# Optimization experiments

Measured on AMD Instinct MI355X. Metric: run time of the kernel, lower is better.

## Reference

```python
import jax, jax.numpy as jnp
import numpy as np

N = 50000
E = 800000
IN = 256
H = 8
D = 32
NEG_SLOPE = 0.2


def setup_inputs() -> dict:
    key = jax.random.key(0)
    ks = jax.random.split(key, 16)
    inp = {
        "h": jax.random.normal(ks[0], (N, IN), jnp.float32),
        "src_a": jax.random.randint(ks[1], (E,), 0, N),
        "dst_a": jax.random.randint(ks[2], (E,), 0, N),
        "src_b": jax.random.randint(ks[3], (E,), 0, N),
        "dst_b": jax.random.randint(ks[4], (E,), 0, N),
        "W_a": jax.random.normal(ks[5], (IN, H * D), jnp.float32) * 0.05,
        "attn_l_a": jax.random.normal(ks[6], (H, D), jnp.float32) * 0.1,
        "attn_r_a": jax.random.normal(ks[7], (H, D), jnp.float32) * 0.1,
        "bias_a": jax.random.normal(ks[8], (H * D,), jnp.float32) * 0.1,
        "W_b": jax.random.normal(ks[9], (IN, H * D), jnp.float32) * 0.05,
        "attn_l_b": jax.random.normal(ks[10], (H, D), jnp.float32) * 0.1,
        "attn_r_b": jax.random.normal(ks[11], (H, D), jnp.float32) * 0.1,
        "bias_b": jax.random.normal(ks[12], (H * D,), jnp.float32) * 0.1,
        "sem_W1": jax.random.normal(ks[13], (H * D, 128), jnp.float32) * 0.05,
        "sem_b1": jnp.zeros((128,), jnp.float32),
        "sem_W2": jax.random.normal(ks[14], (128, 1), jnp.float32) * 0.1,
    }
    return inp


def gat_conv(h, src, dst, W, attn_l, attn_r, bias):
    # DGL GATConv: project, per-edge additive attention, segment softmax over dst, scatter-agg, bias, ELU
    feat = (h @ W).reshape(N, H, D)                      # [N,H,D]
    el = (feat * attn_l).sum(-1)                          # [N,H]
    er = (feat * attn_r).sum(-1)                          # [N,H]
    e = el[src] + er[dst]                                 # [E,H]
    e = jnp.where(e > 0, e, NEG_SLOPE * e)                # LeakyReLU(0.2)
    m = jax.ops.segment_max(e, dst, num_segments=N)       # [N,H] (-inf for empty)
    ex = jnp.exp(e - m[dst])                              # [E,H]
    denom = jax.ops.segment_sum(ex, dst, num_segments=N)  # [N,H]
    msg = feat[src] * ex[:, :, None]                      # [E,H,D]
    agg = jax.ops.segment_sum(msg, dst, num_segments=N)   # [N,H,D]
    safe = jnp.where(denom > 0, denom, 1.0)
    rst = agg / safe[:, :, None] + bias.reshape(1, H, D)
    rst = jnp.where(rst > 0, rst, jnp.expm1(rst))         # ELU
    return rst.reshape(N, H * D)


def semantic_attention(z, sem_W1, sem_b1, sem_W2):
    # z: [N, M, H*D]
    w = (jnp.tanh(z @ sem_W1 + sem_b1) @ sem_W2).mean(0)  # [M,1]
    beta = jax.nn.softmax(w, axis=0)                      # [M,1]
    return (beta[None] * z).sum(1)                        # [N, H*D]


def reference(h, src_a, dst_a, src_b, dst_b,
              W_a, attn_l_a, attn_r_a, bias_a,
              W_b, attn_l_b, attn_r_b, bias_b,
              sem_W1, sem_b1, sem_W2):
    z_a = gat_conv(h, src_a, dst_a, W_a, attn_l_a, attn_r_a, bias_a)
    z_b = gat_conv(h, src_b, dst_b, W_b, attn_l_b, attn_r_b, bias_b)
    z = jnp.stack([z_a, z_b], axis=1)                     # [N,2,H*D]
    return semantic_attention(z, sem_W1, sem_b1, sem_W2)
```

## Files before the change

kernel.cpp:

```cpp
#include <hip/hip_runtime.h>
#include <math.h>

typedef __attribute__((ext_vector_type(8))) short bf16x8;
typedef __attribute__((ext_vector_type(4))) float f32x4;
typedef __attribute__((ext_vector_type(4))) unsigned short us4;
typedef __attribute__((ext_vector_type(8))) unsigned short us8;

static constexpr int kN  = 50000;
static constexpr int kE  = 800000;
static constexpr int kNBUK = 98;
static constexpr int kCAP  = 9216;

__device__ __forceinline__ float b2f(unsigned short u) {
  union { unsigned u; float f; } x; x.u = ((unsigned)u) << 16; return x.f;
}
__device__ __forceinline__ unsigned short f2b(float f) {
  union { float f; unsigned u; } x; x.f = f;
  unsigned u = x.u;
  unsigned r = (u + 0x7fffu + ((u >> 16) & 1u)) >> 16;
  return (unsigned short)r;
}

__global__ __launch_bounds__(256)
void k_prep(const float* __restrict__ Wa, const float* __restrict__ Wb,
            const float* __restrict__ W1,
            unsigned short* __restrict__ wta, unsigned short* __restrict__ wtb,
            unsigned short* __restrict__ w1t) {
  int b = blockIdx.x, t = threadIdx.x;
  if (b < 256) {
    int i = b * 256 + t, j = i >> 8, k = i & 255;
    wta[j * 256 + k] = f2b(Wa[k * 256 + j]);
  } else if (b < 512) {
    int i = (b - 256) * 256 + t, j = i >> 8, k = i & 255;
    wtb[j * 256 + k] = f2b(Wb[k * 256 + j]);
  } else {
    int i = (b - 512) * 256 + t, j = i >> 8, k = i & 255;
    w1t[j * 256 + k] = f2b(W1[k * 128 + j]);
  }
}

__global__ __launch_bounds__(512, 4)
void k_gemm(const float* __restrict__ h,
            const unsigned short* __restrict__ wta,
            const unsigned short* __restrict__ wtb,
            const float* __restrict__ ala, const float* __restrict__ ara,
            const float* __restrict__ alb, const float* __restrict__ arb,
            unsigned short* __restrict__ fa, unsigned short* __restrict__ fb,
            float* __restrict__ ela, float* __restrict__ era,
            float* __restrict__ elb, float* __restrict__ erb) {
  __shared__ us8 la[128 * 8];
  __shared__ us8 lb[256 * 8];
  const int z = blockIdx.y;
  const unsigned short* wt = z ? wtb : wta;
  unsigned short* f = z ? fb : fa;
  const float* al = z ? alb : ala;
  const float* ar = z ? arb : ara;
  float* el = z ? elb : ela;
  float* er = z ? erb : era;
  const int m0 = blockIdx.x * 128;
  const int t = threadIdx.x;
  const int lane = t & 63;
  const int wave = t >> 6;
  const int col = lane & 15;
  const int quad = lane >> 4;
  const int mw = (wave >> 2) * 64;
  const int nw = (wave & 3) * 64;
  f32x4 acc[4][4];
#pragma unroll
  for (int i = 0; i < 4; ++i)
#pragma unroll
    for (int j = 0; j < 4; ++j) acc[i][j] = (f32x4){0.f, 0.f, 0.f, 0.f};

  for (int ks = 0; ks < 4; ++ks) {
    const int k0 = ks * 64;
    __syncthreads();
#pragma unroll
    for (int i = 0; i < 4; ++i) {
      int idx = i * 512 + t;
      int r = idx >> 4, g = (idx >> 1) & 7, half = idx & 1;
      int gr = m0 + r;
      f32x4 v = {0.f, 0.f, 0.f, 0.f};
      if (gr < kN) v = *(const f32x4*)(h + (size_t)gr * 256 + k0 + g * 8 + half * 4);
      us4 o;
      o.x = f2b(v.x); o.y = f2b(v.y); o.z = f2b(v.z); o.w = f2b(v.w);
      *(us4*)((unsigned short*)&la[r * 8 + (g ^ (r & 7))] + half * 4) = o;
    }
#pragma unroll
    for (int i = 0; i < 4; ++i) {
      int idx = i * 512 + t;
      int r = idx >> 3, g = idx & 7;
      lb[r * 8 + (g ^ (r & 7))] = *(const us8*)(wt + r * 256 + k0 + g * 8);
    }
    __syncthreads();
#pragma unroll
    for (int k32 = 0; k32 < 64; k32 += 32) {
      const int cg = (k32 >> 3) + quad;
      bf16x8 af[4], bf[4];
#pragma unroll
      for (int s = 0; s < 4; ++s) {
        int arow = mw + s * 16 + col;
        af[s] = (bf16x8)la[arow * 8 + (cg ^ (arow & 7))];
        int brow = nw + s * 16 + col;
        bf[s] = (bf16x8)lb[brow * 8 + (cg ^ (brow & 7))];
      }
#pragma unroll
      for (int i = 0; i < 4; ++i)
#pragma unroll
        for (int j = 0; j < 4; ++j)
          acc[i][j] = __builtin_amdgcn_mfma_f32_16x16x32_bf16(af[i], bf[j],
                                                              acc[i][j], 0, 0, 0);
    }
  }
#pragma unroll
  for (int i = 0; i < 4; ++i) {
#pragma unroll
    for (int r = 0; r < 4; ++r) {
      int row = m0 + mw + i * 16 + quad * 4 + r;
      if (row < kN) {
#pragma unroll
        for (int j = 0; j < 4; ++j)
          f[(size_t)row * 256 + nw + j * 16 + col] = f2b(acc[i][j][r]);
      }
    }
  }
  float alv[4], arv[4];
#pragma unroll
  for (int j = 0; j < 4; ++j) {
    alv[j] = al[nw + j * 16 + col];
    arv[j] = ar[nw + j * 16 + col];
  }
  const int hA = nw >> 5;
#pragma unroll
  for (int i = 0; i < 4; ++i) {
#pragma unroll
    for (int r = 0; r < 4; ++r) {
      float pAl = acc[i][0][r] * alv[0] + acc[i][1][r] * alv[1];
      float pBl = acc[i][2][r] * alv[2] + acc[i][3][r] * alv[3];
      float pAr = acc[i][0][r] * arv[0] + acc[i][1][r] * arv[1];
      float pBr = acc[i][2][r] * arv[2] + acc[i][3][r] * arv[3];
#pragma unroll
      for (int off = 1; off < 16; off <<= 1) {
        pAl += __shfl_xor(pAl, off);
        pBl += __shfl_xor(pBl, off);
        pAr += __shfl_xor(pAr, off);
        pBr += __shfl_xor(pBr, off);
      }
      int row = m0 + mw + i * 16 + quad * 4 + r;
      if (col == 0 && row < kN) {
        el[row * 8 + hA] = pAl;
        el[row * 8 + hA + 1] = pBl;
        er[row * 8 + hA] = pAr;
        er[row * 8 + hA + 1] = pBr;
      }
    }
  }
}

__global__ __launch_bounds__(256)
void k_part(const int* __restrict__ sa, const int* __restrict__ da,
            const int* __restrict__ sb, const int* __restrict__ db,
            int* __restrict__ cnt, unsigned* __restrict__ pay) {
  int y = blockIdx.y;
  const int* s = y ? sb : sa;
  const int* d = y ? db : da;
  unsigned* p = pay + (size_t)y * kNBUK * kCAP;
  int* cn = cnt + y * kNBUK;
  __shared__ unsigned stash[6400];
  __shared__ int h[kNBUK];
  int t = threadIdx.x;
  if (t < kNBUK) h[t] = 0;
  __syncthreads();
  int e0 = blockIdx.x * 6400;
#pragma unroll 5
  for (int it = 0; it < 25; ++it) {
    int e = e0 + it * 256 + t;
    int sv = s[e], dv = d[e];
    int b = dv >> 9;
    stash[it * 256 + t] = (unsigned)sv | ((unsigned)(dv & 511) << 16) |
                          ((unsigned)b << 25);
    atomicAdd(&h[b], 1);
  }
  __syncthreads();
  if (t < kNBUK) h[t] = atomicAdd(&cn[t], h[t]);
  __syncthreads();
#pragma unroll 5
  for (int it = 0; it < 25; ++it) {
    unsigned w = stash[it * 256 + t];
    int b = w >> 25;
    int slot = atomicAdd(&h[b], 1);
    p[b * kCAP + slot] = w & 0x1FFFFFFu;
  }
}

__global__ __launch_bounds__(256)
void k_bscan(const int* __restrict__ cnt, int* __restrict__ bbase,
             int* __restrict__ rpa, int* __restrict__ rpb) {
  __shared__ int buf[2][128];
  int t = threadIdx.x;
  int y = t >> 7, i = t & 127;
  int x = (i < kNBUK) ? cnt[y * kNBUK + i] : 0;
  buf[y][i] = x;
  __syncthreads();
  for (int off = 1; off < 128; off <<= 1) {
    int v = (i >= off) ? buf[y][i - off] : 0;
    __syncthreads();
    buf[y][i] += v;
    __syncthreads();
  }
  if (i < kNBUK) bbase[y * kNBUK + i] = buf[y][i] - x;
  if (t == 0) { rpa[kN] = kE; rpb[kN] = kE; }
}

__global__ __launch_bounds__(256)
void k_bucket(const int* __restrict__ cnt, const int* __restrict__ bbase,
              const unsigned* __restrict__ pay,
              int* __restrict__ rpa, int* __restrict__ rpb,
              int* __restrict__ esa, int* __restrict__ esb) {
  int b = blockIdx.x, y = blockIdx.y;
  int* rp = y ? rpb : rpa;
  int* es = y ? esb : esa;
  const unsigned* p = pay + ((size_t)y * kNBUK + b) * kCAP;
  int c = cnt[y * kNBUK + b];
  int base = bbase[y * kNBUK + b];
  __shared__ unsigned pl[kCAP];
  __shared__ int h[512];
  __shared__ int buf[256];
  int t = threadIdx.x;
  h[t] = 0; h[t + 256] = 0;
  __syncthreads();
  for (int i = t; i < c; i += 256) {
    unsigned w = p[i];
    pl[i] = w;
    atomicAdd(&h[(w >> 16) & 511], 1);
  }
  __syncthreads();
  int a = h[2 * t], b1 = h[2 * t + 1];
  int s2 = a + b1;
  buf[t] = s2;
  __syncthreads();
  for (int off = 1; off < 256; off <<= 1) {
    int v = (t >= off) ? buf[t - off] : 0;
    __syncthreads();
    buf[t] += v;
    __syncthreads();
  }
  int ex = buf[t] - s2;
  int g0 = b * 512 + 2 * t;
  if (g0 < kN) rp[g0] = base + ex;
  if (g0 + 1 < kN) rp[g0 + 1] = base + ex + a;
  h[2 * t] = ex;
  h[2 * t + 1] = ex + a;
  __syncthreads();
  for (int i = t; i < c; i += 256) {
    unsigned w = pl[i];
    int slot = atomicAdd(&h[(w >> 16) & 511], 1);
    es[base + slot] = (int)(w & 0xFFFFu);
  }
}

__global__ __launch_bounds__(256)
void k_agg(const int* __restrict__ rpa, const int* __restrict__ rpb,
           const int* __restrict__ esa, const int* __restrict__ esb,
           const float* __restrict__ ela, const float* __restrict__ era,
           const float* __restrict__ elb, const float* __restrict__ erb,
           const unsigned short* __restrict__ fa,
           const unsigned short* __restrict__ fb,
           const float* __restrict__ biasa, const float* __restrict__ biasb,
           float* __restrict__ za, unsigned short* __restrict__ zb) {
  __shared__ float wls[4][512];
  __shared__ int sls[4][64];
  int bx = blockIdx.x;
  int y = bx >= 12500;
  int nb = y ? bx - 12500 : bx;
  const int* rp = y ? rpb : rpa;
  const int* es = y ? esb : esa;
  const float* el = y ? elb : ela;
  const float* er = y ? erb : era;
  const unsigned short* feat = y ? fb : fa;
  const float* bias = y ? biasb : biasa;
  int lane = threadIdx.x & 63;
  int wave = threadIdx.x >> 6;
  int n = nb * 4 + wave;
  int hh = lane >> 3;
  int h = lane & 7;
  unsigned idxb = (unsigned)lane * 8u;
  float erh = er[n * 8 + h];
  int e0 = rp[n], e1 = rp[n + 1];
  float dsum = 0.f;
  float a0 = 0.f, a1 = 0.f, a2 = 0.f, a3 = 0.f;

  for (int cb = e0; cb < e1; cb += 64) {
    int cnt = e1 - cb;
    if (cnt > 64) cnt = 64;
    for (int it = 0; it * 8 < cnt; ++it) {
      int j = it * 8 + hh;
      if (j < cnt) {
        int s = es[cb + j];
        float ev = *(const float*)((const char*)el + ((unsigned)s << 5) +
                                   ((unsigned)h << 2)) + erh;
        ev = fmaxf(ev, 0.2f * ev);
        float w = __expf(ev);
        wls[wave][it * 64 + lane] = w;
        if (h == 0) sls[wave][j] = s;
        dsum += w;
      }
    }
    int j = 0;
    for (; j + 3 < cnt; j += 4) {
      int s0 = sls[wave][j], s1 = sls[wave][j + 1];
      int s2 = sls[wave][j + 2], s3 = sls[wave][j + 3];
      float w0 = wls[wave][j * 8 + hh];
      float w1 = wls[wave][j * 8 + 8 + hh];
      float w2 = wls[wave][j * 8 + 16 + hh];
      float w3 = wls[wave][j * 8 + 24 + hh];
      us4 f0 = *(const us4*)((const char*)feat + (((unsigned)s0 << 9) + idxb));
      us4 f1 = *(const us4*)((const char*)feat + (((unsigned)s1 << 9) + idxb));
      us4 f2 = *(const us4*)((const char*)feat + (((unsigned)s2 << 9) + idxb));
      us4 f3 = *(const us4*)((const char*)feat + (((unsigned)s3 << 9) + idxb));
      a0 += w0 * b2f(f0.x) + w1 * b2f(f1.x) + w2 * b2f(f2.x) + w3 * b2f(f3.x);
      a1 += w0 * b2f(f0.y) + w1 * b2f(f1.y) + w2 * b2f(f2.y) + w3 * b2f(f3.y);
      a2 += w0 * b2f(f0.z) + w1 * b2f(f1.z) + w2 * b2f(f2.z) + w3 * b2f(f3.z);
      a3 += w0 * b2f(f0.w) + w1 * b2f(f1.w) + w2 * b2f(f2.w) + w3 * b2f(f3.w);
    }
    for (; j < cnt; ++j) {
      int s0 = sls[wave][j];
      float w0 = wls[wave][j * 8 + hh];
      us4 f0 = *(const us4*)((const char*)feat + (((unsigned)s0 << 9) + idxb));
      a0 += w0 * b2f(f0.x);
      a1 += w0 * b2f(f0.y);
      a2 += w0 * b2f(f0.z);
      a3 += w0 * b2f(f0.w);
    }
  }
  dsum += __shfl_xor(dsum, 8);
  dsum += __shfl_xor(dsum, 16);
  dsum += __shfl_xor(dsum, 32);
  float dh = __shfl(dsum, hh);
  float inv = 1.f / (dh > 0.f ? dh : 1.f);
  f32x4 b4 = *(const f32x4*)(bias + lane * 4);
  float r0 = a0 * inv + b4.x;
  float r1 = a1 * inv + b4.y;
  float r2 = a2 * inv + b4.z;
  float r3 = a3 * inv + b4.w;
  r0 = r0 > 0.f ? r0 : expm1f(r0);
  r1 = r1 > 0.f ? r1 : expm1f(r1);
  r2 = r2 > 0.f ? r2 : expm1f(r2);
  r3 = r3 > 0.f ? r3 : expm1f(r3);
  if (y == 0) {
    f32x4 o = {r0, r1, r2, r3};
    *(f32x4*)(za + n * 256 + lane * 4) = o;
  } else {
    us4 o;
    o.x = f2b(r0); o.y = f2b(r1); o.z = f2b(r2); o.w = f2b(r3);
    *(us4*)(zb + n * 256 + lane * 4) = o;
  }
}

__global__ __launch_bounds__(256)
void k_sem(const float* __restrict__ za,
           const unsigned short* __restrict__ zb,
           const unsigned short* __restrict__ w1t,
           const float* __restrict__ b1,
           const float* __restrict__ W2,
           float* __restrict__ wacc) {
  __shared__ us8 w1l[4096];
  int t = threadIdx.x;
  for (int i = t; i < 4096; i += 256) {
    int j = i >> 5, c = i & 31;
    w1l[j * 32 + (c ^ (j & 7))] = ((const us8*)w1t)[i];
  }
  __syncthreads();
  int lane = t & 63, wave = t >> 6;
  int col = lane & 15, quad = lane >> 4;
  float b1v[8], w2v[8];
#pragma unroll
  for (int tt = 0; tt < 8; ++tt) {
    b1v[tt] = b1[tt * 16 + col];
    w2v[tt] = W2[tt * 16 + col];
  }
  int gw = blockIdx.x * 4 + wave;
  int nw = gridDim.x * 4;
  float sa = 0.f, sb = 0.f;
  for (int gt = gw; gt < 6250; gt += nw) {
    f32x4 acc[8];
#pragma unroll
    for (int tt = 0; tt < 8; ++tt) acc[tt] = (f32x4){0.f, 0.f, 0.f, 0.f};
#pragma unroll
    for (int ks = 0; ks < 8; ++ks) {
      bf16x8 a;
      if (gt < 3125) {
        const float* ap = za + (size_t)gt * 4096 + col * 256 + ks * 32 + quad * 8;
        f32x4 a0 = *(const f32x4*)ap;
        f32x4 a1 = *(const f32x4*)(ap + 4);
        a[0] = (short)f2b(a0.x); a[1] = (short)f2b(a0.y);
        a[2] = (short)f2b(a0.z); a[3] = (short)f2b(a0.w);
        a[4] = (short)f2b(a1.x); a[5] = (short)f2b(a1.y);
        a[6] = (short)f2b(a1.z); a[7] = (short)f2b(a1.w);
      } else {
        a = *(const bf16x8*)(zb + (size_t)(gt - 3125) * 4096 + col * 256 +
                             ks * 32 + quad * 8);
      }
      int c = ks * 4 + quad;
#pragma unroll
      for (int tt = 0; tt < 8; ++tt) {
        int j = tt * 16 + col;
        bf16x8 b = (bf16x8)w1l[j * 32 + (c ^ (j & 7))];
        acc[tt] = __builtin_amdgcn_mfma_f32_16x16x32_bf16(a, b, acc[tt], 0, 0, 0);
      }
    }
    float tot = 0.f;
#pragma unroll
    for (int tt = 0; tt < 8; ++tt)
#pragma unroll
      for (int r = 0; r < 4; ++r)
        tot += tanhf(acc[tt][r] + b1v[tt]) * w2v[tt];
#pragma unroll
    for (int off = 1; off < 64; off <<= 1) tot += __shfl_xor(tot, off);
    if (gt < 3125) sa += tot; else sb += tot;
  }
  if (lane == 0) {
    if (sa != 0.f) atomicAdd(&wacc[0], sa);
    if (sb != 0.f) atomicAdd(&wacc[1], sb);
  }
}

__global__ __launch_bounds__(256)
void k_combine(const float* __restrict__ za,
               const unsigned short* __restrict__ zb,
               const float* __restrict__ wacc,
               float* __restrict__ out) {
  int i = blockIdx.x * 256 + threadIdx.x;
  float wa = wacc[0] * (1.f / kN), wb = wacc[1] * (1.f / kN);
  float mx = fmaxf(wa, wb);
  float ea = __expf(wa - mx), eb = __expf(wb - mx);
  float inv = 1.f / (ea + eb);
  float ba = ea * inv, bb = eb * inv;
  f32x4 x = ((const f32x4*)za)[i];
  us4 yv = ((const us4*)zb)[i];
  f32x4 o;
#pragma unroll
  for (int j = 0; j < 4; ++j)
    o[j] = ba * x[j] + bb * b2f(yv[j]);
  ((f32x4*)out)[i] = o;
}

extern "C" void kernel_launch(void* const* d_in, const int* in_sizes, int n_in,
                              void* d_out, int out_size, void* d_ws, size_t ws_size,
                              hipStream_t stream) {
  const float* hin = (const float*)d_in[0];
  const int* src_a = (const int*)d_in[1];
  const int* dst_a = (const int*)d_in[2];
  const int* src_b = (const int*)d_in[3];
  const int* dst_b = (const int*)d_in[4];
  const float* W_a = (const float*)d_in[5];
  const float* al_a = (const float*)d_in[6];
  const float* ar_a = (const float*)d_in[7];
  const float* bias_a = (const float*)d_in[8];
  const float* W_b = (const float*)d_in[9];
  const float* al_b = (const float*)d_in[10];
  const float* ar_b = (const float*)d_in[11];
  const float* bias_b = (const float*)d_in[12];
  const float* sW1 = (const float*)d_in[13];
  const float* sb1 = (const float*)d_in[14];
  const float* sW2 = (const float*)d_in[15];
  float* out = (float*)d_out;

  char* wsb = (char*)d_ws;
  size_t off = 0;
  auto alloc = [&](size_t bytes) -> char* {
    char* p = wsb + off;
    off = (off + bytes + 511) & ~(size_t)511;
    return p;
  };
  unsigned short* feat_a = (unsigned short*)alloc((size_t)kN * 256 * 2);
  unsigned short* feat_b = (unsigned short*)alloc((size_t)kN * 256 * 2);
  unsigned short* z_b    = (unsigned short*)alloc((size_t)kN * 256 * 2);
  float* el_a = (float*)alloc((size_t)kN * 8 * 4);
  float* er_a = (float*)alloc((size_t)kN * 8 * 4);
  float* el_b = (float*)alloc((size_t)kN * 8 * 4);
  float* er_b = (float*)alloc((size_t)kN * 8 * 4);
  unsigned short* wt_a = (unsigned short*)alloc(65536 * 2);
  unsigned short* wt_b = (unsigned short*)alloc(65536 * 2);
  unsigned short* w1t  = (unsigned short*)alloc(32768 * 2);
  int* rp_a = (int*)alloc((size_t)(kN + 1) * 4);
  int* rp_b = (int*)alloc((size_t)(kN + 1) * 4);
  int* es_a = (int*)alloc((size_t)kE * 4);
  int* es_b = (int*)alloc((size_t)kE * 4);
  unsigned* pay = (unsigned*)alloc((size_t)2 * kNBUK * kCAP * 4);
  int* cnt = (int*)alloc((size_t)2 * kNBUK * 4);
  int* bbase = (int*)alloc((size_t)2 * kNBUK * 4);
  float* wacc = (float*)alloc(2 * 4);

  hipMemsetAsync(cnt, 0, (size_t)2 * kNBUK * 4, stream);
  hipMemsetAsync(wacc, 0, 8, stream);

  k_prep<<<640, 256, 0, stream>>>(W_a, W_b, sW1, wt_a, wt_b, w1t);
  k_part<<<dim3(125, 2), 256, 0, stream>>>(src_a, dst_a, src_b, dst_b, cnt, pay);
  k_bscan<<<1, 256, 0, stream>>>(cnt, bbase, rp_a, rp_b);
  k_bucket<<<dim3(kNBUK, 2), 256, 0, stream>>>(cnt, bbase, pay,
                                               rp_a, rp_b, es_a, es_b);
  k_gemm<<<dim3(391, 2), 512, 0, stream>>>(hin, wt_a, wt_b,
                                           al_a, ar_a, al_b, ar_b,
                                           feat_a, feat_b,
                                           el_a, er_a, el_b, er_b);
  k_agg<<<25000, 256, 0, stream>>>(rp_a, rp_b, es_a, es_b,
                                   el_a, er_a, el_b, er_b,
                                   feat_a, feat_b, bias_a, bias_b,
                                   out, z_b);
  k_sem<<<512, 256, 0, stream>>>(out, z_b, w1t, sb1, sW2, wacc);
  k_combine<<<12500, 256, 0, stream>>>(out, z_b, wacc, out);
}
```

Before: 453.0 us.

## Widen feature gathers to 16-byte loads with half-wave edge split; use fast tanh/rcp

```diff
diff --git a/kernel.cpp b/kernel.cpp
--- a/kernel.cpp
+++ b/kernel.cpp
@@ -283,11 +283,15 @@
   int n = nb * 4 + wave;
   int hh = lane >> 3;
   int h = lane & 7;
-  unsigned idxb = (unsigned)lane * 8u;
+  int half = lane >> 5;
+  int l5 = lane & 31;
+  int h2 = l5 >> 2;
+  unsigned idx16 = (unsigned)l5 * 16u;
   float erh = er[n * 8 + h];
   int e0 = rp[n], e1 = rp[n + 1];
   float dsum = 0.f;
   float a0 = 0.f, a1 = 0.f, a2 = 0.f, a3 = 0.f;
+  float a4 = 0.f, a5 = 0.f, a6 = 0.f, a7 = 0.f;
 
   for (int cb = e0; cb < e1; cb += 64) {
     int cnt = e1 - cb;
@@ -306,53 +310,79 @@
       }
     }
     int j = 0;
-    for (; j + 3 < cnt; j += 4) {
-      int s0 = sls[wave][j], s1 = sls[wave][j + 1];
-      int s2 = sls[wave][j + 2], s3 = sls[wave][j + 3];
-      float w0 = wls[wave][j * 8 + hh];
-      float w1 = wls[wave][j * 8 + 8 + hh];
-      float w2 = wls[wave][j * 8 + 16 + hh];
-      float w3 = wls[wave][j * 8 + 24 + hh];
-      us4 f0 = *(const us4*)((const char*)feat + (((unsigned)s0 << 9) + idxb));
-      us4 f1 = *(const us4*)((const char*)feat + (((unsigned)s1 << 9) + idxb));
-      us4 f2 = *(const us4*)((const char*)feat + (((unsigned)s2 << 9) + idxb));
-      us4 f3 = *(const us4*)((const char*)feat + (((unsigned)s3 << 9) + idxb));
-      a0 += w0 * b2f(f0.x) + w1 * b2f(f1.x) + w2 * b2f(f2.x) + w3 * b2f(f3.x);
-      a1 += w0 * b2f(f0.y) + w1 * b2f(f1.y) + w2 * b2f(f2.y) + w3 * b2f(f3.y);
-      a2 += w0 * b2f(f0.z) + w1 * b2f(f1.z) + w2 * b2f(f2.z) + w3 * b2f(f3.z);
-      a3 += w0 * b2f(f0.w) + w1 * b2f(f1.w) + w2 * b2f(f2.w) + w3 * b2f(f3.w);
-    }
-    for (; j < cnt; ++j) {
-      int s0 = sls[wave][j];
-      float w0 = wls[wave][j * 8 + hh];
-      us4 f0 = *(const us4*)((const char*)feat + (((unsigned)s0 << 9) + idxb));
-      a0 += w0 * b2f(f0.x);
-      a1 += w0 * b2f(f0.y);
-      a2 += w0 * b2f(f0.z);
-      a3 += w0 * b2f(f0.w);
-    }
-  }
+    for (; j + 7 < cnt; j += 8) {
+#pragma unroll
+      for (int p = 0; p < 4; ++p) {
+        int jj = j + 2 * p + half;
+        int s = sls[wave][jj];
+        float w = wls[wave][jj * 8 + h2];
+        us8 fv = *(const us8*)((const char*)feat + (((unsigned)s << 9) + idx16));
+        a0 += w * b2f(fv[0]);
+        a1 += w * b2f(fv[1]);
+        a2 += w * b2f(fv[2]);
+        a3 += w * b2f(fv[3]);
+        a4 += w * b2f(fv[4]);
+        a5 += w * b2f(fv[5]);
+        a6 += w * b2f(fv[6]);
+        a7 += w * b2f(fv[7]);
+      }
+    }
+    if (j < cnt) {
+#pragma unroll
+      for (int p = 0; p < 4; ++p) {
+        int jj = j + 2 * p + half;
+        bool v = jj < cnt;
+        int jc = v ? jj : j;
+        int s = sls[wave][jc];
+        float w = v ? wls[wave][jc * 8 + h2] : 0.f;
+        us8 fv = *(const us8*)((const char*)feat + (((unsigned)s << 9) + idx16));
+        a0 += w * b2f(fv[0]);
+        a1 += w * b2f(fv[1]);
+        a2 += w * b2f(fv[2]);
+        a3 += w * b2f(fv[3]);
+        a4 += w * b2f(fv[4]);
+        a5 += w * b2f(fv[5]);
+        a6 += w * b2f(fv[6]);
+        a7 += w * b2f(fv[7]);
+      }
+    }
+  }
+  a0 += __shfl_xor(a0, 32); a1 += __shfl_xor(a1, 32);
+  a2 += __shfl_xor(a2, 32); a3 += __shfl_xor(a3, 32);
+  a4 += __shfl_xor(a4, 32); a5 += __shfl_xor(a5, 32);
+  a6 += __shfl_xor(a6, 32); a7 += __shfl_xor(a7, 32);
   dsum += __shfl_xor(dsum, 8);
   dsum += __shfl_xor(dsum, 16);
   dsum += __shfl_xor(dsum, 32);
-  float dh = __shfl(dsum, hh);
-  float inv = 1.f / (dh > 0.f ? dh : 1.f);
-  f32x4 b4 = *(const f32x4*)(bias + lane * 4);
-  float r0 = a0 * inv + b4.x;
-  float r1 = a1 * inv + b4.y;
-  float r2 = a2 * inv + b4.z;
-  float r3 = a3 * inv + b4.w;
-  r0 = r0 > 0.f ? r0 : expm1f(r0);
-  r1 = r1 > 0.f ? r1 : expm1f(r1);
-  r2 = r2 > 0.f ? r2 : expm1f(r2);
-  r3 = r3 > 0.f ? r3 : expm1f(r3);
+  float dh = __shfl(dsum, h2);
+  float inv = __builtin_amdgcn_rcpf(dh > 0.f ? dh : 1.f);
+  f32x4 blo = *(const f32x4*)(bias + l5 * 8);
+  f32x4 bhi = *(const f32x4*)(bias + l5 * 8 + 4);
+  float r0 = a0 * inv + blo.x;
+  float r1 = a1 * inv + blo.y;
+  float r2 = a2 * inv + blo.z;
+  float r3 = a3 * inv + blo.w;
+  float r4 = a4 * inv + bhi.x;
+  float r5 = a5 * inv + bhi.y;
+  float r6 = a6 * inv + bhi.z;
+  float r7 = a7 * inv + bhi.w;
+  r0 = r0 > 0.f ? r0 : __expf(r0) - 1.f;
+  r1 = r1 > 0.f ? r1 : __expf(r1) - 1.f;
+  r2 = r2 > 0.f ? r2 : __expf(r2) - 1.f;
+  r3 = r3 > 0.f ? r3 : __expf(r3) - 1.f;
+  r4 = r4 > 0.f ? r4 : __expf(r4) - 1.f;
+  r5 = r5 > 0.f ? r5 : __expf(r5) - 1.f;
+  r6 = r6 > 0.f ? r6 : __expf(r6) - 1.f;
+  r7 = r7 > 0.f ? r7 : __expf(r7) - 1.f;
+  f32x4 lo = {r0, r1, r2, r3};
+  f32x4 hi = {r4, r5, r6, r7};
+  f32x4 ov = half ? hi : lo;
   if (y == 0) {
-    f32x4 o = {r0, r1, r2, r3};
-    *(f32x4*)(za + n * 256 + lane * 4) = o;
+    *(f32x4*)((char*)za + (size_t)n * 1024 + l5 * 32 + half * 16) = ov;
   } else {
     us4 o;
-    o.x = f2b(r0); o.y = f2b(r1); o.z = f2b(r2); o.w = f2b(r3);
-    *(us4*)(zb + n * 256 + lane * 4) = o;
+    o.x = f2b(ov.x); o.y = f2b(ov.y); o.z = f2b(ov.z); o.w = f2b(ov.w);
+    *(us4*)((char*)zb + (size_t)n * 512 + l5 * 16 + half * 8) = o;
   }
 }
 
@@ -412,8 +442,12 @@
 #pragma unroll
     for (int tt = 0; tt < 8; ++tt)
 #pragma unroll
-      for (int r = 0; r < 4; ++r)
-        tot += tanhf(acc[tt][r] + b1v[tt]) * w2v[tt];
+      for (int r = 0; r < 4; ++r) {
+        float x = acc[tt][r] + b1v[tt];
+        x = fminf(fmaxf(x, -10.f), 10.f);
+        float ex = __expf(2.f * x);
+        tot += (ex - 1.f) * __builtin_amdgcn_rcpf(ex + 1.f) * w2v[tt];
+      }
 #pragma unroll
     for (int off = 1; off < 64; off <<= 1) tot += __shfl_xor(tot, off);
     if (gt < 3125) sa += tot; else sb += tot;
@@ -433,7 +467,7 @@
   float wa = wacc[0] * (1.f / kN), wb = wacc[1] * (1.f / kN);
   float mx = fmaxf(wa, wb);
   float ea = __expf(wa - mx), eb = __expf(wb - mx);
-  float inv = 1.f / (ea + eb);
+  float inv = __builtin_amdgcn_rcpf(ea + eb);
   float ba = ea * inv, bb = eb * inv;
   f32x4 x = ((const f32x4*)za)[i];
   us4 yv = ((const us4*)zb)[i];
```

Result: no change. 447.3 us (-1.2%).

## Process two destination nodes per wave with 16-byte feature gathers in aggregation

Applied to the files above, without the earlier changes.

```diff
diff --git a/kernel.cpp b/kernel.cpp
--- a/kernel.cpp
+++ b/kernel.cpp
@@ -267,11 +267,11 @@
            const unsigned short* __restrict__ fb,
            const float* __restrict__ biasa, const float* __restrict__ biasb,
            float* __restrict__ za, unsigned short* __restrict__ zb) {
-  __shared__ float wls[4][512];
-  __shared__ int sls[4][64];
+  __shared__ float wls[4][2][256];
+  __shared__ int sls[4][2][32];
   int bx = blockIdx.x;
-  int y = bx >= 12500;
-  int nb = y ? bx - 12500 : bx;
+  int y = bx >= 6250;
+  int nb = y ? bx - 6250 : bx;
   const int* rp = y ? rpb : rpa;
   const int* es = y ? esb : esa;
   const float* el = y ? elb : ela;
@@ -280,79 +280,166 @@
   const float* bias = y ? biasb : biasa;
   int lane = threadIdx.x & 63;
   int wave = threadIdx.x >> 6;
-  int n = nb * 4 + wave;
+  int nA = nb * 8 + wave * 2;
+  int nB = nA + 1;
   int hh = lane >> 3;
   int h = lane & 7;
-  unsigned idxb = (unsigned)lane * 8u;
-  float erh = er[n * 8 + h];
-  int e0 = rp[n], e1 = rp[n + 1];
-  float dsum = 0.f;
-  float a0 = 0.f, a1 = 0.f, a2 = 0.f, a3 = 0.f;
-
-  for (int cb = e0; cb < e1; cb += 64) {
-    int cnt = e1 - cb;
-    if (cnt > 64) cnt = 64;
-    for (int it = 0; it * 8 < cnt; ++it) {
+  int half = lane >> 5;
+  int l5 = lane & 31;
+  int h2 = l5 >> 2;
+  unsigned idx16 = (unsigned)l5 * 16u;
+  float erhA = er[nA * 8 + h];
+  float erhB = er[nB * 8 + h];
+  int e0A = rp[nA], e1A = rp[nA + 1], e1B = rp[nB + 1];
+  int cbA = e0A, cbB = e1A;
+  float dsumA = 0.f, dsumB = 0.f;
+  float aA0 = 0.f, aA1 = 0.f, aA2 = 0.f, aA3 = 0.f;
+  float aA4 = 0.f, aA5 = 0.f, aA6 = 0.f, aA7 = 0.f;
+  float aB0 = 0.f, aB1 = 0.f, aB2 = 0.f, aB3 = 0.f;
+  float aB4 = 0.f, aB5 = 0.f, aB6 = 0.f, aB7 = 0.f;
+
+  while (cbA < e1A || cbB < e1B) {
+    int cntA = e1A - cbA; cntA = cntA < 0 ? 0 : (cntA > 32 ? 32 : cntA);
+    int cntB = e1B - cbB; cntB = cntB < 0 ? 0 : (cntB > 32 ? 32 : cntB);
+#pragma unroll
+    for (int it = 0; it < 4; ++it) {
       int j = it * 8 + hh;
-      if (j < cnt) {
-        int s = es[cb + j];
-        float ev = *(const float*)((const char*)el + ((unsigned)s << 5) +
-                                   ((unsigned)h << 2)) + erh;
-        ev = fmaxf(ev, 0.2f * ev);
-        float w = __expf(ev);
-        wls[wave][it * 64 + lane] = w;
-        if (h == 0) sls[wave][j] = s;
-        dsum += w;
-      }
-    }
-    int j = 0;
-    for (; j + 3 < cnt; j += 4) {
-      int s0 = sls[wave][j], s1 = sls[wave][j + 1];
-      int s2 = sls[wave][j + 2], s3 = sls[wave][j + 3];
-      float w0 = wls[wave][j * 8 + hh];
-      float w1 = wls[wave][j * 8 + 8 + hh];
-      float w2 = wls[wave][j * 8 + 16 + hh];
-      float w3 = wls[wave][j * 8 + 24 + hh];
-      us4 f0 = *(const us4*)((const char*)feat + (((unsigned)s0 << 9) + idxb));
-      us4 f1 = *(const us4*)((const char*)feat + (((unsigned)s1 << 9) + idxb));
-      us4 f2 = *(const us4*)((const char*)feat + (((unsigned)s2 << 9) + idxb));
-      us4 f3 = *(const us4*)((const char*)feat + (((unsigned)s3 << 9) + idxb));
-      a0 += w0 * b2f(f0.x) + w1 * b2f(f1.x) + w2 * b2f(f2.x) + w3 * b2f(f3.x);
-      a1 += w0 * b2f(f0.y) + w1 * b2f(f1.y) + w2 * b2f(f2.y) + w3 * b2f(f3.y);
-      a2 += w0 * b2f(f0.z) + w1 * b2f(f1.z) + w2 * b2f(f2.z) + w3 * b2f(f3.z);
-      a3 += w0 * b2f(f0.w) + w1 * b2f(f1.w) + w2 * b2f(f2.w) + w3 * b2f(f3.w);
-    }
-    for (; j < cnt; ++j) {
-      int s0 = sls[wave][j];
-      float w0 = wls[wave][j * 8 + hh];
-      us4 f0 = *(const us4*)((const char*)feat + (((unsigned)s0 << 9) + idxb));
-      a0 += w0 * b2f(f0.x);
-      a1 += w0 * b2f(f0.y);
-      a2 += w0 * b2f(f0.z);
-      a3 += w0 * b2f(f0.w);
-    }
-  }
-  dsum += __shfl_xor(dsum, 8);
-  dsum += __shfl_xor(dsum, 16);
-  dsum += __shfl_xor(dsum, 32);
-  float dh = __shfl(dsum, hh);
-  float inv = 1.f / (dh > 0.f ? dh : 1.f);
-  f32x4 b4 = *(const f32x4*)(bias + lane * 4);
-  float r0 = a0 * inv + b4.x;
-  float r1 = a1 * inv + b4.y;
-  float r2 = a2 * inv + b4.z;
-  float r3 = a3 * inv + b4.w;
-  r0 = r0 > 0.f ? r0 : expm1f(r0);
-  r1 = r1 > 0.f ? r1 : expm1f(r1);
-  r2 = r2 > 0.f ? r2 : expm1f(r2);
-  r3 = r3 > 0.f ? r3 : expm1f(r3);
+      bool vA = j < cntA, vB = j < cntB;
+      int sA = vA ? es[cbA + j] : 0;
+      int sB = vB ? es[cbB + j] : 0;
+      float xA = vA ? *(const float*)((const char*)el + ((unsigned)sA << 5) +
+                                      ((unsigned)h << 2)) : 0.f;
+      float xB = vB ? *(const float*)((const char*)el + ((unsigned)sB << 5) +
+                                      ((unsigned)h << 2)) : 0.f;
+      float eA = xA + erhA, eB = xB + erhB;
+      eA = fmaxf(eA, 0.2f * eA);
+      eB = fmaxf(eB, 0.2f * eB);
+      float wA = __expf(eA), wB = __expf(eB);
+      wls[wave][0][it * 64 + lane] = wA;
+      wls[wave][1][it * 64 + lane] = wB;
+      if (vA) dsumA += wA;
+      if (vB) dsumB += wB;
+      if (h == 0) {
+        if (vA) sls[wave][0][j] = sA;
+        if (vB) sls[wave][1][j] = sB;
+      }
+    }
+    int jmax = cntA > cntB ? cntA : cntB;
+    for (int j = 0; j < jmax; j += 4) {
+      bool dA0 = j < cntA, dA1 = j + 2 < cntA;
+      bool dB0 = j < cntB, dB1 = j + 2 < cntB;
+      float wA0, wA1, wB0, wB1;
+      us8 fA0, fA1, fB0, fB1;
+      if (dA0) {
+        int jj = j + half; bool v = jj < cntA; int jc = v ? jj : j;
+        int s = sls[wave][0][jc];
+        wA0 = v ? wls[wave][0][jc * 8 + h2] : 0.f;
+        fA0 = *(const us8*)((const char*)feat + (((unsigned)s << 9) + idx16));
+      }
+      if (dA1) {
+        int jj = j + 2 + half; bool v = jj < cntA; int jc = v ? jj : j + 2;
+        int s = sls[wave][0][jc];
+        wA1 = v ? wls[wave][0][jc * 8 + h2] : 0.f;
+        fA1 = *(const us8*)((const char*)feat + (((unsigned)s << 9) + idx16));
+      }
+      if (dB0) {
+        int jj = j + half; bool v = jj < cntB; int jc = v ? jj : j;
+        int s = sls[wave][1][jc];
+        wB0 = v ? wls[wave][1][jc * 8 + h2] : 0.f;
+        fB0 = *(const us8*)((const char*)feat + (((unsigned)s << 9) + idx16));
+      }
+      if (dB1) {
+        int jj = j + 2 + half; bool v = jj < cntB; int jc = v ? jj : j + 2;
+        int s = sls[wave][1][jc];
+        wB1 = v ? wls[wave][1][jc * 8 + h2] : 0.f;
+        fB1 = *(const us8*)((const char*)feat + (((unsigned)s << 9) + idx16));
+      }
+      if (dA0) {
+        aA0 += wA0 * b2f(fA0[0]); aA1 += wA0 * b2f(fA0[1]);
+        aA2 += wA0 * b2f(fA0[2]); aA3 += wA0 * b2f(fA0[3]);
+        aA4 += wA0 * b2f(fA0[4]); aA5 += wA0 * b2f(fA0[5]);
+        aA6 += wA0 * b2f(fA0[6]); aA7 += wA0 * b2f(fA0[7]);
+      }
+      if (dA1) {
+        aA0 += wA1 * b2f(fA1[0]); aA1 += wA1 * b2f(fA1[1]);
+        aA2 += wA1 * b2f(fA1[2]); aA3 += wA1 * b2f(fA1[3]);
+        aA4 += wA1 * b2f(fA1[4]); aA5 += wA1 * b2f(fA1[5]);
+        aA6 += wA1 * b2f(fA1[6]); aA7 += wA1 * b2f(fA1[7]);
+      }
+      if (dB0) {
+        aB0 += wB0 * b2f(fB0[0]); aB1 += wB0 * b2f(fB0[1]);
+        aB2 += wB0 * b2f(fB0[2]); aB3 += wB0 * b2f(fB0[3]);
+        aB4 += wB0 * b2f(fB0[4]); aB5 += wB0 * b2f(fB0[5]);
+        aB6 += wB0 * b2f(fB0[6]); aB7 += wB0 * b2f(fB0[7]);
+      }
+      if (dB1) {
+        aB0 += wB1 * b2f(fB1[0]); aB1 += wB1 * b2f(fB1[1]);
+        aB2 += wB1 * b2f(fB1[2]); aB3 += wB1 * b2f(fB1[3]);
+        aB4 += wB1 * b2f(fB1[4]); aB5 += wB1 * b2f(fB1[5]);
+        aB6 += wB1 * b2f(fB1[6]); aB7 += wB1 * b2f(fB1[7]);
+      }
+    }
+    cbA += 32; cbB += 32;
+  }
+  aA0 += __shfl_xor(aA0, 32); aA1 += __shfl_xor(aA1, 32);
+  aA2 += __shfl_xor(aA2, 32); aA3 += __shfl_xor(aA3, 32);
+  aA4 += __shfl_xor(aA4, 32); aA5 += __shfl_xor(aA5, 32);
+  aA6 += __shfl_xor(aA6, 32); aA7 += __shfl_xor(aA7, 32);
+  aB0 += __shfl_xor(aB0, 32); aB1 += __shfl_xor(aB1, 32);
+  aB2 += __shfl_xor(aB2, 32); aB3 += __shfl_xor(aB3, 32);
+  aB4 += __shfl_xor(aB4, 32); aB5 += __shfl_xor(aB5, 32);
+  aB6 += __shfl_xor(aB6, 32); aB7 += __shfl_xor(aB7, 32);
+  dsumA += __shfl_xor(dsumA, 8);
+  dsumA += __shfl_xor(dsumA, 16);
+  dsumA += __shfl_xor(dsumA, 32);
+  dsumB += __shfl_xor(dsumB, 8);
+  dsumB += __shfl_xor(dsumB, 16);
+  dsumB += __shfl_xor(dsumB, 32);
+  float dhA = __shfl(dsumA, h2);
+  float dhB = __shfl(dsumB, h2);
+  float invA = __builtin_amdgcn_rcpf(dhA > 0.f ? dhA : 1.f);
+  float invB = __builtin_amdgcn_rcpf(dhB > 0.f ? dhB : 1.f);
+  f32x4 blo = *(const f32x4*)(bias + l5 * 8);
+  f32x4 bhi = *(const f32x4*)(bias + l5 * 8 + 4);
+  float rA0 = aA0 * invA + blo.x, rA1 = aA1 * invA + blo.y;
+  float rA2 = aA2 * invA + blo.z, rA3 = aA3 * invA + blo.w;
+  float rA4 = aA4 * invA + bhi.x, rA5 = aA5 * invA + bhi.y;
+  float rA6 = aA6 * invA + bhi.z, rA7 = aA7 * invA + bhi.w;
+  float rB0 = aB0 * invB + blo.x, rB1 = aB1 * invB + blo.y;
+  float rB2 = aB2 * invB + blo.z, rB3 = aB3 * invB + blo.w;
+  float rB4 = aB4 * invB + bhi.x, rB5 = aB5 * invB + bhi.y;
+  float rB6 = aB6 * invB + bhi.z, rB7 = aB7 * invB + bhi.w;
+  rA0 = rA0 > 0.f ? rA0 : __expf(rA0) - 1.f;
+  rA1 = rA1 > 0.f ? rA1 : __expf(rA1) - 1.f;
+  rA2 = rA2 > 0.f ? rA2 : __expf(rA2) - 1.f;
+  rA3 = rA3 > 0.f ? rA3 : __expf(rA3) - 1.f;
+  rA4 = rA4 > 0.f ? rA4 : __expf(rA4) - 1.f;
+  rA5 = rA5 > 0.f ? rA5 : __expf(rA5) - 1.f;
+  rA6 = rA6 > 0.f ? rA6 : __expf(rA6) - 1.f;
+  rA7 = rA7 > 0.f ? rA7 : __expf(rA7) - 1.f;
+  rB0 = rB0 > 0.f ? rB0 : __expf(rB0) - 1.f;
+  rB1 = rB1 > 0.f ? rB1 : __expf(rB1) - 1.f;
+  rB2 = rB2 > 0.f ? rB2 : __expf(rB2) - 1.f;
+  rB3 = rB3 > 0.f ? rB3 : __expf(rB3) - 1.f;
+  rB4 = rB4 > 0.f ? rB4 : __expf(rB4) - 1.f;
+  rB5 = rB5 > 0.f ? rB5 : __expf(rB5) - 1.f;
+  rB6 = rB6 > 0.f ? rB6 : __expf(rB6) - 1.f;
+  rB7 = rB7 > 0.f ? rB7 : __expf(rB7) - 1.f;
+  f32x4 loA = {rA0, rA1, rA2, rA3};
+  f32x4 hiA = {rA4, rA5, rA6, rA7};
+  f32x4 loB = {rB0, rB1, rB2, rB3};
+  f32x4 hiB = {rB4, rB5, rB6, rB7};
+  f32x4 ovA = half ? hiA : loA;
+  f32x4 ovB = half ? hiB : loB;
   if (y == 0) {
-    f32x4 o = {r0, r1, r2, r3};
-    *(f32x4*)(za + n * 256 + lane * 4) = o;
+    *(f32x4*)((char*)za + (size_t)nA * 1024 + l5 * 32 + half * 16) = ovA;
+    *(f32x4*)((char*)za + (size_t)nB * 1024 + l5 * 32 + half * 16) = ovB;
   } else {
-    us4 o;
-    o.x = f2b(r0); o.y = f2b(r1); o.z = f2b(r2); o.w = f2b(r3);
-    *(us4*)(zb + n * 256 + lane * 4) = o;
+    us4 oA, oB;
+    oA.x = f2b(ovA.x); oA.y = f2b(ovA.y); oA.z = f2b(ovA.z); oA.w = f2b(ovA.w);
+    oB.x = f2b(ovB.x); oB.y = f2b(ovB.y); oB.z = f2b(ovB.z); oB.w = f2b(ovB.w);
+    *(us4*)((char*)zb + (size_t)nA * 512 + l5 * 16 + half * 8) = oA;
+    *(us4*)((char*)zb + (size_t)nB * 512 + l5 * 16 + half * 8) = oB;
   }
 }
 
@@ -412,8 +499,12 @@
 #pragma unroll
     for (int tt = 0; tt < 8; ++tt)
 #pragma unroll
-      for (int r = 0; r < 4; ++r)
-        tot += tanhf(acc[tt][r] + b1v[tt]) * w2v[tt];
+      for (int r = 0; r < 4; ++r) {
+        float x = acc[tt][r] + b1v[tt];
+        x = fminf(fmaxf(x, -10.f), 10.f);
+        float ex = __expf(2.f * x);
+        tot += (ex - 1.f) * __builtin_amdgcn_rcpf(ex + 1.f) * w2v[tt];
+      }
 #pragma unroll
     for (int off = 1; off < 64; off <<= 1) tot += __shfl_xor(tot, off);
     if (gt < 3125) sa += tot; else sb += tot;
@@ -433,7 +524,7 @@
   float wa = wacc[0] * (1.f / kN), wb = wacc[1] * (1.f / kN);
   float mx = fmaxf(wa, wb);
   float ea = __expf(wa - mx), eb = __expf(wb - mx);
-  float inv = 1.f / (ea + eb);
+  float inv = __builtin_amdgcn_rcpf(ea + eb);
   float ba = ea * inv, bb = eb * inv;
   f32x4 x = ((const f32x4*)za)[i];
   us4 yv = ((const us4*)zb)[i];
@@ -503,7 +594,7 @@
                                            al_a, ar_a, al_b, ar_b,
                                            feat_a, feat_b,
                                            el_a, er_a, el_b, er_b);
-  k_agg<<<25000, 256, 0, stream>>>(rp_a, rp_b, es_a, es_b,
+  k_agg<<<12500, 256, 0, stream>>>(rp_a, rp_b, es_a, es_b,
                                    el_a, er_a, el_b, er_b,
                                    feat_a, feat_b, bias_a, bias_b,
                                    out, z_b);
```

Measured after the change: 462.4 us. +2.1%, slower.

## Split GAT aggregation per head across blocks and use fast tanh/rcp intrinsics

Applied to the files above, without the earlier changes.

```diff
diff --git a/kernel.cpp b/kernel.cpp
--- a/kernel.cpp
+++ b/kernel.cpp
@@ -267,11 +267,11 @@
            const unsigned short* __restrict__ fb,
            const float* __restrict__ biasa, const float* __restrict__ biasb,
            float* __restrict__ za, unsigned short* __restrict__ zb) {
-  __shared__ float wls[4][512];
-  __shared__ int sls[4][64];
-  int bx = blockIdx.x;
-  int y = bx >= 12500;
-  int nb = y ? bx - 12500 : bx;
+  int b = blockIdx.x;
+  int y = b >= 100000;
+  if (y) b -= 100000;
+  int h = b & 7;
+  int g = b >> 3;
   const int* rp = y ? rpb : rpa;
   const int* es = y ? esb : esa;
   const float* el = y ? elb : ela;
@@ -280,79 +280,66 @@
   const float* bias = y ? biasb : biasa;
   int lane = threadIdx.x & 63;
   int wave = threadIdx.x >> 6;
-  int n = nb * 4 + wave;
-  int hh = lane >> 3;
-  int h = lane & 7;
-  unsigned idxb = (unsigned)lane * 8u;
+  int n = g * 4 + wave;
+  int e3 = lane >> 3;
+  int d = lane & 7;
   float erh = er[n * 8 + h];
   int e0 = rp[n], e1 = rp[n + 1];
   float dsum = 0.f;
-  float a0 = 0.f, a1 = 0.f, a2 = 0.f, a3 = 0.f;
+  f32x4 acc = {0.f, 0.f, 0.f, 0.f};
+  unsigned doff = (unsigned)h * 64u + (unsigned)d * 8u;
 
   for (int cb = e0; cb < e1; cb += 64) {
     int cnt = e1 - cb;
     if (cnt > 64) cnt = 64;
+    float wreg = 0.f;
+    int sreg = 0;
+    if (lane < cnt) {
+      sreg = es[cb + lane];
+      float ev = el[sreg * 8 + h] + erh;
+      ev = fmaxf(ev, 0.2f * ev);
+      wreg = __expf(ev);
+      dsum += wreg;
+    }
     for (int it = 0; it * 8 < cnt; ++it) {
-      int j = it * 8 + hh;
-      if (j < cnt) {
-        int s = es[cb + j];
-        float ev = *(const float*)((const char*)el + ((unsigned)s << 5) +
-                                   ((unsigned)h << 2)) + erh;
-        ev = fmaxf(ev, 0.2f * ev);
-        float w = __expf(ev);
-        wls[wave][it * 64 + lane] = w;
-        if (h == 0) sls[wave][j] = s;
-        dsum += w;
-      }
-    }
-    int j = 0;
-    for (; j + 3 < cnt; j += 4) {
-      int s0 = sls[wave][j], s1 = sls[wave][j + 1];
-      int s2 = sls[wave][j + 2], s3 = sls[wave][j + 3];
-      float w0 = wls[wave][j * 8 + hh];
-      float w1 = wls[wave][j * 8 + 8 + hh];
-      float w2 = wls[wave][j * 8 + 16 + hh];
-      float w3 = wls[wave][j * 8 + 24 + hh];
-      us4 f0 = *(const us4*)((const char*)feat + (((unsigned)s0 << 9) + idxb));
-      us4 f1 = *(const us4*)((const char*)feat + (((unsigned)s1 << 9) + idxb));
-      us4 f2 = *(const us4*)((const char*)feat + (((unsigned)s2 << 9) + idxb));
-      us4 f3 = *(const us4*)((const char*)feat + (((unsigned)s3 << 9) + idxb));
-      a0 += w0 * b2f(f0.x) + w1 * b2f(f1.x) + w2 * b2f(f2.x) + w3 * b2f(f3.x);
-      a1 += w0 * b2f(f0.y) + w1 * b2f(f1.y) + w2 * b2f(f2.y) + w3 * b2f(f3.y);
-      a2 += w0 * b2f(f0.z) + w1 * b2f(f1.z) + w2 * b2f(f2.z) + w3 * b2f(f3.z);
-      a3 += w0 * b2f(f0.w) + w1 * b2f(f1.w) + w2 * b2f(f2.w) + w3 * b2f(f3.w);
-    }
-    for (; j < cnt; ++j) {
-      int s0 = sls[wave][j];
-      float w0 = wls[wave][j * 8 + hh];
-      us4 f0 = *(const us4*)((const char*)feat + (((unsigned)s0 << 9) + idxb));
-      a0 += w0 * b2f(f0.x);
-      a1 += w0 * b2f(f0.y);
-      a2 += w0 * b2f(f0.z);
-      a3 += w0 * b2f(f0.w);
-    }
-  }
-  dsum += __shfl_xor(dsum, 8);
-  dsum += __shfl_xor(dsum, 16);
-  dsum += __shfl_xor(dsum, 32);
-  float dh = __shfl(dsum, hh);
-  float inv = 1.f / (dh > 0.f ? dh : 1.f);
-  f32x4 b4 = *(const f32x4*)(bias + lane * 4);
-  float r0 = a0 * inv + b4.x;
-  float r1 = a1 * inv + b4.y;
-  float r2 = a2 * inv + b4.z;
-  float r3 = a3 * inv + b4.w;
-  r0 = r0 > 0.f ? r0 : expm1f(r0);
-  r1 = r1 > 0.f ? r1 : expm1f(r1);
-  r2 = r2 > 0.f ? r2 : expm1f(r2);
-  r3 = r3 > 0.f ? r3 : expm1f(r3);
-  if (y == 0) {
-    f32x4 o = {r0, r1, r2, r3};
-    *(f32x4*)(za + n * 256 + lane * 4) = o;
-  } else {
-    us4 o;
-    o.x = f2b(r0); o.y = f2b(r1); o.z = f2b(r2); o.w = f2b(r3);
-    *(us4*)(zb + n * 256 + lane * 4) = o;
+      int j = it * 8 + e3;
+      float w = __shfl(wreg, j);
+      int s = __shfl(sreg, j);
+      us4 fv = *(const us4*)((const char*)feat + ((unsigned)s << 9) + doff);
+      acc.x += w * b2f(fv.x);
+      acc.y += w * b2f(fv.y);
+      acc.z += w * b2f(fv.z);
+      acc.w += w * b2f(fv.w);
+    }
+  }
+#pragma unroll
+  for (int off = 8; off <= 32; off <<= 1) {
+    acc.x += __shfl_xor(acc.x, off);
+    acc.y += __shfl_xor(acc.y, off);
+    acc.z += __shfl_xor(acc.z, off);
+    acc.w += __shfl_xor(acc.w, off);
+  }
+#pragma unroll
+  for (int off = 1; off < 64; off <<= 1) dsum += __shfl_xor(dsum, off);
+  float inv = __builtin_amdgcn_rcpf(dsum > 0.f ? dsum : 1.f);
+  f32x4 b4 = *(const f32x4*)(bias + h * 32 + d * 4);
+  float r0 = acc.x * inv + b4.x;
+  float r1 = acc.y * inv + b4.y;
+  float r2 = acc.z * inv + b4.z;
+  float r3 = acc.w * inv + b4.w;
+  r0 = r0 > 0.f ? r0 : __expf(r0) - 1.f;
+  r1 = r1 > 0.f ? r1 : __expf(r1) - 1.f;
+  r2 = r2 > 0.f ? r2 : __expf(r2) - 1.f;
+  r3 = r3 > 0.f ? r3 : __expf(r3) - 1.f;
+  if (lane < 8) {
+    if (y == 0) {
+      f32x4 o = {r0, r1, r2, r3};
+      *(f32x4*)(za + (size_t)n * 256 + h * 32 + lane * 4) = o;
+    } else {
+      us4 o;
+      o.x = f2b(r0); o.y = f2b(r1); o.z = f2b(r2); o.w = f2b(r3);
+      *(us4*)(zb + (size_t)n * 256 + h * 32 + lane * 4) = o;
+    }
   }
 }
 
@@ -412,8 +399,12 @@
 #pragma unroll
     for (int tt = 0; tt < 8; ++tt)
 #pragma unroll
-      for (int r = 0; r < 4; ++r)
-        tot += tanhf(acc[tt][r] + b1v[tt]) * w2v[tt];
+      for (int r = 0; r < 4; ++r) {
+        float x = acc[tt][r] + b1v[tt];
+        x = fminf(fmaxf(x, -10.f), 10.f);
+        float ex = __expf(2.f * x);
+        tot += (ex - 1.f) * __builtin_amdgcn_rcpf(ex + 1.f) * w2v[tt];
+      }
 #pragma unroll
     for (int off = 1; off < 64; off <<= 1) tot += __shfl_xor(tot, off);
     if (gt < 3125) sa += tot; else sb += tot;
@@ -433,7 +424,7 @@
   float wa = wacc[0] * (1.f / kN), wb = wacc[1] * (1.f / kN);
   float mx = fmaxf(wa, wb);
   float ea = __expf(wa - mx), eb = __expf(wb - mx);
-  float inv = 1.f / (ea + eb);
+  float inv = __builtin_amdgcn_rcpf(ea + eb);
   float ba = ea * inv, bb = eb * inv;
   f32x4 x = ((const f32x4*)za)[i];
   us4 yv = ((const us4*)zb)[i];
@@ -503,10 +494,10 @@
                                            al_a, ar_a, al_b, ar_b,
                                            feat_a, feat_b,
                                            el_a, er_a, el_b, er_b);
-  k_agg<<<25000, 256, 0, stream>>>(rp_a, rp_b, es_a, es_b,
-                                   el_a, er_a, el_b, er_b,
-                                   feat_a, feat_b, bias_a, bias_b,
-                                   out, z_b);
+  k_agg<<<200000, 256, 0, stream>>>(rp_a, rp_b, es_a, es_b,
+                                    el_a, er_a, el_b, er_b,
+                                    feat_a, feat_b, bias_a, bias_b,
+                                    out, z_b);
   k_sem<<<512, 256, 0, stream>>>(out, z_b, w1t, sb1, sW2, wacc);
   k_combine<<<12500, 256, 0, stream>>>(out, z_b, wacc, out);
 }
```

Result: slower. 656.8 us (+45.0%).
